# Kernel optimization log

Measured on AMD Instinct MI355X. Metric: run time of the kernel, lower is better.

Reference implementation:

```python
import jax, jax.numpy as jnp
import numpy as np

NUM_EMBEDDINGS = 1024
EMBEDDING_DIM = 64
BETA = 0.25


def setup_inputs() -> dict:
    key = jax.random.key(0)
    k1, k2 = jax.random.split(key)
    z = jax.random.normal(k1, (16, EMBEDDING_DIM, 64, 64), dtype=jnp.float32)
    # matches torch init: uniform_(-1/K, 1/K)
    lim = 1.0 / NUM_EMBEDDINGS
    embedding = jax.random.uniform(k2, (NUM_EMBEDDINGS, EMBEDDING_DIM),
                                   dtype=jnp.float32, minval=-lim, maxval=lim)
    return {"z": z, "embedding": embedding}


def reference(z, embedding):
    B, C, H, W = z.shape  # C == EMBEDDING_DIM
    # [B,C,H,W] -> [B*H*W, C]
    z_flat = jnp.transpose(z, (0, 2, 3, 1)).reshape(-1, C)
    # squared euclidean distances (argmin-equivalent to torch.cdist):
    # ||z||^2 - 2 z.e + ||e||^2 ; shape [N, K]
    d = (jnp.sum(z_flat * z_flat, axis=-1, keepdims=True)
         - 2.0 * (z_flat @ embedding.T)
         + jnp.sum(embedding * embedding, axis=-1))
    encoding_indices = jnp.argmin(d, axis=1)  # [N] int
    z_q_flat = embedding[encoding_indices]    # gather [N, C]
    z_q = jnp.transpose(z_q_flat.reshape(B, H, W, C), (0, 3, 1, 2))
    vq_loss = jnp.mean(jnp.square(jax.lax.stop_gradient(z_q) - z))
    commitment_loss = BETA * jnp.mean(jnp.square(jax.lax.stop_gradient(z) - z_q))
    return (z_q, encoding_indices, vq_loss + commitment_loss)
```

## Files before the change

kernel.cpp:

```cpp
#include <hip/hip_runtime.h>

#define N_PIX   65536
#define CDIM    64
#define KCODES  1024
#define HWSZ    4096
#define KCHUNK  128
#define NCHUNK  8
#define TPB     256

#define OFF_NE   0
#define OFF_NZ   1024
#define OFF_MIN  66560
#define OFF_IDX  590848
#define OFF_LOSS 1115136

#define OUT_IDX  (N_PIX * CDIM)
#define OUT_LOSS (OUT_IDX + N_PIX)

__device__ __forceinline__ float np_pairwise64(const float* a) {
#pragma clang fp contract(off)
    float r0 = a[0], r1 = a[1], r2 = a[2], r3 = a[3];
    float r4 = a[4], r5 = a[5], r6 = a[6], r7 = a[7];
    for (int i = 8; i < 64; i += 8) {
        r0 += a[i + 0]; r1 += a[i + 1]; r2 += a[i + 2]; r3 += a[i + 3];
        r4 += a[i + 4]; r5 += a[i + 5]; r6 += a[i + 6]; r7 += a[i + 7];
    }
    return ((r0 + r1) + (r2 + r3)) + ((r4 + r5) + (r6 + r7));
}

__global__ void vq_prep(const float* emb, float* ws) {
#pragma clang fp contract(off)
    int k = blockIdx.x * blockDim.x + threadIdx.x;
    if (k == 0) ws[OFF_LOSS] = 0.0f;
    if (k >= KCODES) return;
    float prod[CDIM];
    for (int c = 0; c < CDIM; ++c) {
        float v = emb[k * CDIM + c];
        prod[c] = v * v;
    }
    ws[OFF_NE + k] = np_pairwise64(prod);
}

__global__ __launch_bounds__(TPB) void vq_nz(const float* z, float* ws) {
#pragma clang fp contract(off)
    const int p  = blockIdx.x * TPB + threadIdx.x;
    const int b  = p >> 12;
    const int hw = p & (HWSZ - 1);
    const float* zp = z + ((size_t)(b * CDIM) << 12) + hw;
    float prod[CDIM];
    for (int c = 0; c < CDIM; ++c) {
        float v = zp[(size_t)c << 12];
        prod[c] = v * v;
    }
    ws[OFF_NZ + p] = np_pairwise64(prod);
}

__global__ __launch_bounds__(TPB) void vq_argmin(const float* z, const float* ws,
                                                 const float* emb,
                                                 float* cmin, int* cidx) {
#pragma clang fp contract(off)
    __shared__ float se[KCHUNK * CDIM];
    __shared__ float sn[KCHUNK];

    const int chunk = blockIdx.y;
    const int k0 = chunk * KCHUNK;

    const float4* esrc = (const float4*)(emb + k0 * CDIM);
    float4* edst = (float4*)se;
    for (int i = threadIdx.x; i < KCHUNK * CDIM / 4; i += TPB) edst[i] = esrc[i];
    for (int i = threadIdx.x; i < KCHUNK; i += TPB) sn[i] = ws[OFF_NE + k0 + i];
    __syncthreads();

    const int p  = blockIdx.x * TPB + threadIdx.x;
    const int b  = p >> 12;
    const int hw = p & (HWSZ - 1);

    const float* zp = z + ((size_t)(b * CDIM) << 12) + hw;
    float zr[CDIM];
#pragma unroll
    for (int c = 0; c < CDIM; ++c) zr[c] = zp[(size_t)c << 12];

    const float nz = ws[OFF_NZ + p];

    float best = 3.4e38f;
    int   bi   = k0;
    for (int kk = 0; kk < KCHUNK; kk += 2) {
        const float4* e0 = (const float4*)(se + kk * CDIM);
        const float4* e1 = (const float4*)(se + (kk + 1) * CDIM);
        float a0 = 0.f, a1 = 0.f;
#pragma unroll
        for (int j = 0; j < 16; ++j) {
            float4 v0 = e0[j];
            float4 v1 = e1[j];
            a0 = fmaf(zr[4 * j + 0], v0.x, a0);
            a0 = fmaf(zr[4 * j + 1], v0.y, a0);
            a0 = fmaf(zr[4 * j + 2], v0.z, a0);
            a0 = fmaf(zr[4 * j + 3], v0.w, a0);
            a1 = fmaf(zr[4 * j + 0], v1.x, a1);
            a1 = fmaf(zr[4 * j + 1], v1.y, a1);
            a1 = fmaf(zr[4 * j + 2], v1.z, a1);
            a1 = fmaf(zr[4 * j + 3], v1.w, a1);
        }
        float t0 = nz - 2.0f * a0;
        float d0 = t0 + sn[kk];
        float t1 = nz - 2.0f * a1;
        float d1 = t1 + sn[kk + 1];
        if (d0 < best) { best = d0; bi = k0 + kk; }
        if (d1 < best) { best = d1; bi = k0 + kk + 1; }
    }
    cmin[(p << 3) + chunk] = best;
    cidx[(p << 3) + chunk] = bi;
}

__global__ __launch_bounds__(TPB) void vq_finalize(const float* z, const float* emb,
                                                   const float* cmin, const int* cidx,
                                                   float* out, float* loss_acc) {
    const int p = blockIdx.x * TPB + threadIdx.x;

    float best = cmin[p << 3];
    int   bi   = cidx[p << 3];
#pragma unroll
    for (int ch = 1; ch < NCHUNK; ++ch) {
        float m = cmin[(p << 3) + ch];
        if (m < best) { best = m; bi = cidx[(p << 3) + ch]; }
    }

    out[OUT_IDX + p] = (float)bi;

    const float* ev = emb + bi * CDIM;
    const int b  = p >> 12;
    const int hw = p & (HWSZ - 1);
    const float* zp = z + ((size_t)(b * CDIM) << 12) + hw;
    float* zq = out + ((size_t)(b * CDIM) << 12) + hw;

    float ls = 0.0f;
#pragma unroll
    for (int c = 0; c < CDIM; ++c) {
        float e = ev[c];
        float zv = zp[(size_t)c << 12];
        float d = e - zv;
        ls = fmaf(d, d, ls);
        zq[(size_t)c << 12] = e;
    }

#pragma unroll
    for (int off = 32; off > 0; off >>= 1) ls += __shfl_down(ls, off);
    __shared__ float wsum[TPB / 64];
    if ((threadIdx.x & 63) == 0) wsum[threadIdx.x >> 6] = ls;
    __syncthreads();
    if (threadIdx.x == 0) {
        float s = wsum[0] + wsum[1] + wsum[2] + wsum[3];
        atomicAdd(loss_acc, s);
    }
}

__global__ void vq_loss_out(const float* loss_acc, float* out) {
    out[OUT_LOSS] = loss_acc[0] * (1.25f / (float)(N_PIX * CDIM));
}

extern "C" void kernel_launch(void* const* d_in, const int* in_sizes, int n_in,
                              void* d_out, int out_size, void* d_ws, size_t ws_size,
                              hipStream_t stream) {
    const float* z   = (const float*)d_in[0];
    const float* emb = (const float*)d_in[1];
    float* ws   = (float*)d_ws;
    float* out  = (float*)d_out;
    float* cmin = ws + OFF_MIN;
    int*   cidx = (int*)(ws + OFF_IDX);
    float* lossp = ws + OFF_LOSS;

    vq_prep<<<dim3(KCODES / TPB), dim3(TPB), 0, stream>>>(emb, ws);
    vq_nz<<<dim3(N_PIX / TPB), dim3(TPB), 0, stream>>>(z, ws);
    vq_argmin<<<dim3(N_PIX / TPB, NCHUNK), dim3(TPB), 0, stream>>>(z, ws, emb, cmin, cidx);
    vq_finalize<<<dim3(N_PIX / TPB), dim3(TPB), 0, stream>>>(z, emb, cmin, cidx, out, lossp);
    vq_loss_out<<<1, 1, 0, stream>>>(lossp, out);
}
```

Measured before the change: 226.6 us.

## Fuse z-norm into argmin kernel and read codebook directly from global memory

Removes the separate vq_nz kernel by computing each pixel's squared norm inside vq_argmin from the z values already held in registers. It also drops the shared-memory staging of the codebook chunk and its barrier, so the kernel now reads embedding rows and their norms straight from global memory. Since every thread reads the same address, these become uniform or broadcast loads, which may be served as scalar or cached loads. Pointers are marked __restrict__ throughout. The risk is that per-thread global or scalar loads inside the hot loop have more latency than LDS reads, and the z-norm is now computed once for each of the 8 chunks instead of once overall.

```diff
diff --git a/kernel.cpp b/kernel.cpp
--- a/kernel.cpp
+++ b/kernel.cpp
@@ -9,67 +9,38 @@
 #define TPB     256
 
 #define OFF_NE   0
-#define OFF_NZ   1024
-#define OFF_MIN  66560
-#define OFF_IDX  590848
-#define OFF_LOSS 1115136
+#define OFF_MIN  1024
+#define OFF_IDX  525312
+#define OFF_LOSS 1049600
 
 #define OUT_IDX  (N_PIX * CDIM)
 #define OUT_LOSS (OUT_IDX + N_PIX)
 
-__device__ __forceinline__ float np_pairwise64(const float* a) {
-#pragma clang fp contract(off)
-    float r0 = a[0], r1 = a[1], r2 = a[2], r3 = a[3];
-    float r4 = a[4], r5 = a[5], r6 = a[6], r7 = a[7];
-    for (int i = 8; i < 64; i += 8) {
-        r0 += a[i + 0]; r1 += a[i + 1]; r2 += a[i + 2]; r3 += a[i + 3];
-        r4 += a[i + 4]; r5 += a[i + 5]; r6 += a[i + 6]; r7 += a[i + 7];
-    }
-    return ((r0 + r1) + (r2 + r3)) + ((r4 + r5) + (r6 + r7));
-}
-
-__global__ void vq_prep(const float* emb, float* ws) {
+__global__ void vq_prep(const float* __restrict__ emb, float* __restrict__ ws) {
 #pragma clang fp contract(off)
     int k = blockIdx.x * blockDim.x + threadIdx.x;
     if (k == 0) ws[OFF_LOSS] = 0.0f;
     if (k >= KCODES) return;
-    float prod[CDIM];
-    for (int c = 0; c < CDIM; ++c) {
-        float v = emb[k * CDIM + c];
-        prod[c] = v * v;
+    const float* e = emb + k * CDIM;
+    float r0 = e[0]*e[0], r1 = e[1]*e[1], r2 = e[2]*e[2], r3 = e[3]*e[3];
+    float r4 = e[4]*e[4], r5 = e[5]*e[5], r6 = e[6]*e[6], r7 = e[7]*e[7];
+    for (int i = 8; i < CDIM; i += 8) {
+        r0 = r0 + e[i+0]*e[i+0]; r1 = r1 + e[i+1]*e[i+1];
+        r2 = r2 + e[i+2]*e[i+2]; r3 = r3 + e[i+3]*e[i+3];
+        r4 = r4 + e[i+4]*e[i+4]; r5 = r5 + e[i+5]*e[i+5];
+        r6 = r6 + e[i+6]*e[i+6]; r7 = r7 + e[i+7]*e[i+7];
     }
-    ws[OFF_NE + k] = np_pairwise64(prod);
+    ws[OFF_NE + k] = ((r0 + r1) + (r2 + r3)) + ((r4 + r5) + (r6 + r7));
 }
 
-__global__ __launch_bounds__(TPB) void vq_nz(const float* z, float* ws) {
+__global__ __launch_bounds__(TPB) void vq_argmin(const float* __restrict__ z,
+                                                 const float* __restrict__ ws,
+                                                 const float* __restrict__ emb,
+                                                 float* __restrict__ cmin,
+                                                 int* __restrict__ cidx) {
 #pragma clang fp contract(off)
-    const int p  = blockIdx.x * TPB + threadIdx.x;
-    const int b  = p >> 12;
-    const int hw = p & (HWSZ - 1);
-    const float* zp = z + ((size_t)(b * CDIM) << 12) + hw;
-    float prod[CDIM];
-    for (int c = 0; c < CDIM; ++c) {
-        float v = zp[(size_t)c << 12];
-        prod[c] = v * v;
-    }
-    ws[OFF_NZ + p] = np_pairwise64(prod);
-}
-
-__global__ __launch_bounds__(TPB) void vq_argmin(const float* z, const float* ws,
-                                                 const float* emb,
-                                                 float* cmin, int* cidx) {
-#pragma clang fp contract(off)
-    __shared__ float se[KCHUNK * CDIM];
-    __shared__ float sn[KCHUNK];
-
     const int chunk = blockIdx.y;
     const int k0 = chunk * KCHUNK;
-
-    const float4* esrc = (const float4*)(emb + k0 * CDIM);
-    float4* edst = (float4*)se;
-    for (int i = threadIdx.x; i < KCHUNK * CDIM / 4; i += TPB) edst[i] = esrc[i];
-    for (int i = threadIdx.x; i < KCHUNK; i += TPB) sn[i] = ws[OFF_NE + k0 + i];
-    __syncthreads();
 
     const int p  = blockIdx.x * TPB + threadIdx.x;
     const int b  = p >> 12;
@@ -80,13 +51,24 @@
 #pragma unroll
     for (int c = 0; c < CDIM; ++c) zr[c] = zp[(size_t)c << 12];
 
-    const float nz = ws[OFF_NZ + p];
+    float r0 = zr[0]*zr[0], r1 = zr[1]*zr[1], r2 = zr[2]*zr[2], r3 = zr[3]*zr[3];
+    float r4 = zr[4]*zr[4], r5 = zr[5]*zr[5], r6 = zr[6]*zr[6], r7 = zr[7]*zr[7];
+#pragma unroll
+    for (int i = 8; i < CDIM; i += 8) {
+        r0 = r0 + zr[i+0]*zr[i+0]; r1 = r1 + zr[i+1]*zr[i+1];
+        r2 = r2 + zr[i+2]*zr[i+2]; r3 = r3 + zr[i+3]*zr[i+3];
+        r4 = r4 + zr[i+4]*zr[i+4]; r5 = r5 + zr[i+5]*zr[i+5];
+        r6 = r6 + zr[i+6]*zr[i+6]; r7 = r7 + zr[i+7]*zr[i+7];
+    }
+    const float nz = ((r0 + r1) + (r2 + r3)) + ((r4 + r5) + (r6 + r7));
+
+    const float* nep = ws + OFF_NE;
 
     float best = 3.4e38f;
     int   bi   = k0;
     for (int kk = 0; kk < KCHUNK; kk += 2) {
-        const float4* e0 = (const float4*)(se + kk * CDIM);
-        const float4* e1 = (const float4*)(se + (kk + 1) * CDIM);
+        const float4* e0 = (const float4*)(emb + (size_t)(k0 + kk) * CDIM);
+        const float4* e1 = e0 + (CDIM / 4);
         float a0 = 0.f, a1 = 0.f;
 #pragma unroll
         for (int j = 0; j < 16; ++j) {
@@ -102,9 +84,9 @@
             a1 = fmaf(zr[4 * j + 3], v1.w, a1);
         }
         float t0 = nz - 2.0f * a0;
-        float d0 = t0 + sn[kk];
+        float d0 = t0 + nep[k0 + kk];
         float t1 = nz - 2.0f * a1;
-        float d1 = t1 + sn[kk + 1];
+        float d1 = t1 + nep[k0 + kk + 1];
         if (d0 < best) { best = d0; bi = k0 + kk; }
         if (d1 < best) { best = d1; bi = k0 + kk + 1; }
     }
@@ -112,9 +94,12 @@
     cidx[(p << 3) + chunk] = bi;
 }
 
-__global__ __launch_bounds__(TPB) void vq_finalize(const float* z, const float* emb,
-                                                   const float* cmin, const int* cidx,
-                                                   float* out, float* loss_acc) {
+__global__ __launch_bounds__(TPB) void vq_finalize(const float* __restrict__ z,
+                                                   const float* __restrict__ emb,
+                                                   const float* __restrict__ cmin,
+                                                   const int* __restrict__ cidx,
+                                                   float* __restrict__ out,
+                                                   float* __restrict__ loss_acc) {
     const int p = blockIdx.x * TPB + threadIdx.x;
 
     float best = cmin[p << 3];
@@ -154,7 +139,7 @@
     }
 }
 
-__global__ void vq_loss_out(const float* loss_acc, float* out) {
+__global__ void vq_loss_out(const float* __restrict__ loss_acc, float* __restrict__ out) {
     out[OUT_LOSS] = loss_acc[0] * (1.25f / (float)(N_PIX * CDIM));
 }
 
@@ -170,7 +155,6 @@
     float* lossp = ws + OFF_LOSS;
 
     vq_prep<<<dim3(KCODES / TPB), dim3(TPB), 0, stream>>>(emb, ws);
-    vq_nz<<<dim3(N_PIX / TPB), dim3(TPB), 0, stream>>>(z, ws);
     vq_argmin<<<dim3(N_PIX / TPB, NCHUNK), dim3(TPB), 0, stream>>>(z, ws, emb, cmin, cidx);
     vq_finalize<<<dim3(N_PIX / TPB), dim3(TPB), 0, stream>>>(z, emb, cmin, cidx, out, lossp);
     vq_loss_out<<<1, 1, 0, stream>>>(lossp, out);
```

New measurement: 251.5 us. +11.0%, slower.
